# Kernel optimization log

Hardware: AMD Instinct MI355X
Metric: run time of the kernel (lower is better)

Reference implementation:

```python
import jax, jax.numpy as jnp
import numpy as np

C = 36   # num_classes
H = 256  # hidden_dim


def setup_inputs() -> dict:
    key = jax.random.key(0)
    ks = jax.random.split(key, 12)
    B, L, Dl, Dg = 32, 196, 1024, 1024
    s = lambda d: 1.0 / np.sqrt(d)
    return {
        "local_features": jax.random.normal(ks[0], (B, L, Dl), jnp.float32),
        "global_average_pool": jax.random.normal(ks[1], (B, Dg), jnp.float32),
        "Wl": jax.random.normal(ks[2], (Dl, C * H), jnp.float32) * s(Dl),
        "bl": jax.random.normal(ks[3], (C * H,), jnp.float32) * s(Dl),
        "Wg": jax.random.normal(ks[4], (Dg, C * H), jnp.float32) * s(Dg),
        "bg": jax.random.normal(ks[5], (C * H,), jnp.float32) * s(Dg),
        "Wh": jax.random.normal(ks[6], (H, H), jnp.float32) * s(H),
        "bh": jax.random.normal(ks[7], (H,), jnp.float32) * s(H),
        "Wr": jax.random.normal(ks[8], (H, 4), jnp.float32) * s(H),
        "br": jax.random.normal(ks[9], (4,), jnp.float32) * s(H),
        "Wc": jax.random.normal(ks[10], (H, 1), jnp.float32) * s(H),
        "bc": jax.random.normal(ks[11], (1,), jnp.float32) * s(H),
    }


def reference(local_features, global_average_pool, Wl, bl, Wg, bg, Wh, bh, Wr, br, Wc, bc):
    B, L, _ = local_features.shape
    # global projection -> [B, C, H]
    xg = (global_average_pool @ Wg + bg).reshape(B, C, H)
    # local projection -> [B, L, C, H] -> [B, C, L, H]
    xl = (local_features @ Wl + bl).reshape(B, L, C, H).transpose(0, 2, 1, 3)
    # per-class attention scores over locations: [B, C, L]
    dot = jnp.einsum('bch,bclh->bcl', xg, xl)
    attn = jax.nn.softmax(dot, axis=-1)
    # attention-weighted sum over locations: [B, C, H]
    ws = jnp.einsum('bcl,bclh->bch', attn, xl)
    hid = jax.nn.relu(ws @ Wh + bh)
    bbox_coords = (hid @ Wr + br).reshape(B, C * 4)   # [B, 4C]
    bbox_presence = (hid @ Wc + bc)[..., 0]           # [B, C]
    return bbox_coords, bbox_presence
```

## Files before the change

kernel.cpp:

```cpp
#include <hip/hip_runtime.h>
#include <hip/hip_bf16.h>
#include <stdint.h>

#define NCLS 36
#define HDIM 256
#define BSZ  32
#define LLOC 196
#define DIN  1024
#define NCH  9216

#define XG_N 294912
#define SC_N 225792
#define V_N  1179648

__global__ __launch_bounds__(256) void kB_xg_part(
    const float* __restrict__ Wg, const float* __restrict__ gap,
    float* __restrict__ xg_part) {
  __shared__ float4 gs[16][32];
  const int tid = threadIdx.x;
  const int n   = blockIdx.x * 256 + tid;
  const int kc  = blockIdx.y * 128;
  const int b0  = blockIdx.z * 16;

  for (int i = tid; i < 512; i += 256) {
    int bi = i >> 5, pos = i & 31;
    gs[bi][pos] = *(const float4*)&gap[(size_t)(b0 + bi) * DIN + kc + pos * 4];
  }
  __syncthreads();

  float acc[16] = {0,0,0,0,0,0,0,0,0,0,0,0,0,0,0,0};
  const float* wp = Wg + (size_t)kc * NCH + n;
  #pragma unroll 2
  for (int k4 = 0; k4 < 32; ++k4) {
    float w0 = wp[(size_t)(k4 * 4 + 0) * NCH];
    float w1 = wp[(size_t)(k4 * 4 + 1) * NCH];
    float w2 = wp[(size_t)(k4 * 4 + 2) * NCH];
    float w3 = wp[(size_t)(k4 * 4 + 3) * NCH];
    #pragma unroll
    for (int bi = 0; bi < 16; ++bi) {
      float4 g = gs[bi][k4];
      acc[bi] += g.x * w0 + g.y * w1 + g.z * w2 + g.w * w3;
    }
  }
  #pragma unroll
  for (int bi = 0; bi < 16; ++bi)
    xg_part[(size_t)blockIdx.y * XG_N + (size_t)(b0 + bi) * NCH + n] = acc[bi];
}

__global__ void kBr_xg(const float* __restrict__ xg_part,
                       const float* __restrict__ bg, float* __restrict__ xg) {
  int i = blockIdx.x * 256 + threadIdx.x;
  float s = bg[i % NCH];
  #pragma unroll
  for (int p = 0; p < 8; ++p) s += xg_part[(size_t)p * XG_N + i];
  xg[i] = s;
}

__global__ __launch_bounds__(256) void kC_V(
    const float* __restrict__ Wl, const float* __restrict__ xg,
    float* __restrict__ V) {
  __shared__ float4 xs[8][64];
  const int tid = threadIdx.x;
  const int c   = blockIdx.x;
  const int k   = blockIdx.y * 256 + tid;
  const int b0  = blockIdx.z * 8;

  for (int i = tid; i < 512; i += 256) {
    int bi = i >> 6, j = i & 63;
    xs[bi][j] = *(const float4*)&xg[(size_t)(b0 + bi) * NCH + c * HDIM + j * 4];
  }
  __syncthreads();

  float acc[8] = {0,0,0,0,0,0,0,0};
  const float* wl = Wl + (size_t)k * NCH + c * HDIM;
  #pragma unroll 2
  for (int j = 0; j < 64; ++j) {
    float4 w = *(const float4*)&wl[j * 4];
    #pragma unroll
    for (int bi = 0; bi < 8; ++bi) {
      float4 x = xs[bi][j];
      acc[bi] += w.x * x.x + w.y * x.y + w.z * x.z + w.w * x.w;
    }
  }
  #pragma unroll
  for (int bi = 0; bi < 8; ++bi)
    V[(size_t)((b0 + bi) * NCLS + c) * DIN + k] = acc[bi];
}

__global__ __launch_bounds__(256) void kD_scores(
    const float* __restrict__ local, const float* __restrict__ V,
    float* __restrict__ sc_part) {
  __shared__ float4 vs[12][32];
  const int tid = threadIdx.x;
  const int b   = blockIdx.x;
  const int cg  = blockIdx.y;
  const int ks  = blockIdx.z;

  for (int i = tid; i < 384; i += 256) {
    int ci = i >> 5, pos = i & 31;
    vs[ci][pos] = *(const float4*)&V[(size_t)(b * NCLS + cg * 12 + ci) * DIN
                                     + ks * 128 + pos * 4];
  }
  __syncthreads();

  const int l = tid;
  if (l >= LLOC) return;
  const float* lp = local + (size_t)(b * LLOC + l) * DIN + ks * 128;
  float acc[12] = {0,0,0,0,0,0,0,0,0,0,0,0};
  #pragma unroll 2
  for (int j = 0; j < 32; ++j) {
    float4 a = *(const float4*)&lp[j * 4];
    #pragma unroll
    for (int ci = 0; ci < 12; ++ci) {
      float4 v = vs[ci][j];
      acc[ci] += a.x * v.x + a.y * v.y + a.z * v.z + a.w * v.w;
    }
  }
  #pragma unroll
  for (int ci = 0; ci < 12; ++ci)
    sc_part[(size_t)ks * SC_N + (size_t)(b * NCLS + cg * 12 + ci) * LLOC + l] = acc[ci];
}

__global__ __launch_bounds__(64) void kE_softmax(
    const float* __restrict__ sc_part, float* __restrict__ attn2) {
  const int b = blockIdx.x, c = blockIdx.y, t = threadIdx.x;
  const size_t base = (size_t)(b * NCLS + c) * LLOC;
  float sc[4];
  int nl = 0;
  float m = -1e30f;
  for (int l = t; l < LLOC; l += 64) {
    float s = 0.f;
    #pragma unroll
    for (int p = 0; p < 8; ++p) s += sc_part[(size_t)p * SC_N + base + l];
    sc[nl++] = s; m = fmaxf(m, s);
  }
  #pragma unroll
  for (int off = 32; off >= 1; off >>= 1) m = fmaxf(m, __shfl_xor(m, off));
  float sum = 0.f;
  for (int i = 0; i < nl; ++i) { sc[i] = __expf(sc[i] - m); sum += sc[i]; }
  #pragma unroll
  for (int off = 32; off >= 1; off >>= 1) sum += __shfl_xor(sum, off);
  float inv = 1.0f / sum;
  nl = 0;
  for (int l = t; l < LLOC; l += 64) attn2[base + l] = sc[nl++] * inv;
}

__global__ __launch_bounds__(256) void kF_U(
    const float* __restrict__ local, const float* __restrict__ attn2,
    float* __restrict__ U) {
  __shared__ float4 as4[12][49];
  const int tid  = threadIdx.x;
  const int b    = blockIdx.x;
  const int k    = blockIdx.y * 128 + (tid & 127);
  const int half = __builtin_amdgcn_readfirstlane(tid >> 7);
  const int cb   = blockIdx.z * 12;

  for (int i = tid; i < 588; i += 256) {
    int ci = i / 49, pos = i - ci * 49;
    as4[ci][pos] = *(const float4*)&attn2[(size_t)(b * NCLS + cb + ci) * LLOC + pos * 4];
  }
  __syncthreads();

  float acc[6] = {0,0,0,0,0,0};
  const float* lp = local + (size_t)b * LLOC * DIN + k;
  #pragma unroll 2
  for (int l4 = 0; l4 < 49; ++l4) {
    float a0 = lp[(size_t)(l4 * 4 + 0) * DIN];
    float a1 = lp[(size_t)(l4 * 4 + 1) * DIN];
    float a2 = lp[(size_t)(l4 * 4 + 2) * DIN];
    float a3 = lp[(size_t)(l4 * 4 + 3) * DIN];
    #pragma unroll
    for (int ci = 0; ci < 6; ++ci) {
      float4 w = as4[half * 6 + ci][l4];
      acc[ci] += a0 * w.x + a1 * w.y + a2 * w.z + a3 * w.w;
    }
  }
  #pragma unroll
  for (int ci = 0; ci < 6; ++ci)
    U[(size_t)(b * NCLS + cb + half * 6 + ci) * DIN + k] = acc[ci];
}

__global__ __launch_bounds__(256) void kG_ws(
    const float* __restrict__ Wl, const float* __restrict__ U,
    float* __restrict__ wsh_part) {
  __shared__ float4 us[16][32];
  const int tid = threadIdx.x;
  const int c   = blockIdx.x;
  const int kc  = blockIdx.y * 128;
  const int b0  = blockIdx.z * 16;
  const int h   = tid;

  for (int i = tid; i < 512; i += 256) {
    int bi = i >> 5, pos = i & 31;
    us[bi][pos] = *(const float4*)&U[(size_t)((b0 + bi) * NCLS + c) * DIN + kc + pos * 4];
  }
  __syncthreads();

  float acc[16] = {0,0,0,0,0,0,0,0,0,0,0,0,0,0,0,0};
  const float* wp = Wl + (size_t)kc * NCH + c * HDIM + h;
  #pragma unroll 2
  for (int k4 = 0; k4 < 32; ++k4) {
    float w0 = wp[(size_t)(k4 * 4 + 0) * NCH];
    float w1 = wp[(size_t)(k4 * 4 + 1) * NCH];
    float w2 = wp[(size_t)(k4 * 4 + 2) * NCH];
    float w3 = wp[(size_t)(k4 * 4 + 3) * NCH];
    #pragma unroll
    for (int bi = 0; bi < 16; ++bi) {
      float4 u = us[bi][k4];
      acc[bi] += u.x * w0 + u.y * w1 + u.z * w2 + u.w * w3;
    }
  }
  const size_t base = (size_t)blockIdx.y * XG_N + c * HDIM + h;
  #pragma unroll
  for (int bi = 0; bi < 16; ++bi)
    wsh_part[base + (size_t)(b0 + bi) * NCH] = acc[bi];
}

__global__ __launch_bounds__(256) void kH_heads(
    const float* __restrict__ Wh, const float* __restrict__ bh,
    const float* __restrict__ Wr, const float* __restrict__ br,
    const float* __restrict__ Wc, const float* __restrict__ bc,
    const float* __restrict__ bl,
    const float* __restrict__ wsh_part, float* __restrict__ out) {
  __shared__ float ws_s[3][HDIM];
  __shared__ float hid_s[3][HDIM];
  const int b = blockIdx.x, c0 = blockIdx.y * 3;
  const int j = threadIdx.x;

  #pragma unroll
  for (int ci = 0; ci < 3; ++ci) {
    size_t base = (size_t)b * NCH + (c0 + ci) * HDIM + j;
    float s = bl[(c0 + ci) * HDIM + j];
    #pragma unroll
    for (int p = 0; p < 8; ++p) s += wsh_part[(size_t)p * XG_N + base];
    ws_s[ci][j] = s;
  }
  __syncthreads();

  float acc[3] = {0,0,0};
  for (int h = 0; h < HDIM; ++h) {
    float whj = Wh[(size_t)h * HDIM + j];
    acc[0] += ws_s[0][h] * whj;
    acc[1] += ws_s[1][h] * whj;
    acc[2] += ws_s[2][h] * whj;
  }
  float bj = bh[j];
  #pragma unroll
  for (int ci = 0; ci < 3; ++ci) hid_s[ci][j] = fmaxf(acc[ci] + bj, 0.0f);
  __syncthreads();

  const int r = j >> 6, j0 = j & 63;
  for (int ci = 0; ci < 3; ++ci) {
    const int c = c0 + ci;
    float s = 0.f;
    #pragma unroll
    for (int m = 0; m < 4; ++m)
      s += hid_s[ci][j0 + 64 * m] * Wr[(j0 + 64 * m) * 4 + r];
    #pragma unroll
    for (int off = 32; off >= 1; off >>= 1) s += __shfl_xor(s, off);
    if (j0 == 0) out[(size_t)b * (NCLS * 4) + c * 4 + r] = s + br[r];
    if (r == 0) {
      float p = 0.f;
      #pragma unroll
      for (int m = 0; m < 4; ++m)
        p += hid_s[ci][j0 + 64 * m] * Wc[j0 + 64 * m];
      #pragma unroll
      for (int off = 32; off >= 1; off >>= 1) p += __shfl_xor(p, off);
      if (j0 == 0) out[BSZ * NCLS * 4 + b * NCLS + c] = p + bc[0];
    }
  }
}

extern "C" void kernel_launch(void* const* d_in, const int* in_sizes, int n_in,
                              void* d_out, int out_size, void* d_ws, size_t ws_size,
                              hipStream_t stream) {
  const float* local = (const float*)d_in[0];
  const float* gap   = (const float*)d_in[1];
  const float* Wl    = (const float*)d_in[2];
  const float* bl    = (const float*)d_in[3];
  const float* Wg    = (const float*)d_in[4];
  const float* bg    = (const float*)d_in[5];
  const float* Wh    = (const float*)d_in[6];
  const float* bh    = (const float*)d_in[7];
  const float* Wr    = (const float*)d_in[8];
  const float* br    = (const float*)d_in[9];
  const float* Wc    = (const float*)d_in[10];
  const float* bc    = (const float*)d_in[11];
  float* out         = (float*)d_out;

  float* A  = (float*)d_ws;
  float* B  = A + (size_t)8 * XG_N;
  float* C  = B + XG_N;
  float* D  = C + V_N;
  float* E  = D + SC_N;

  kB_xg_part<<<dim3(36, 8, 2), dim3(256), 0, stream>>>(Wg, gap, A);
  kBr_xg   <<<dim3(XG_N / 256), dim3(256), 0, stream>>>(A, bg, B);
  kC_V     <<<dim3(36, 4, 4), dim3(256), 0, stream>>>(Wl, B, C);
  kD_scores<<<dim3(32, 3, 8), dim3(256), 0, stream>>>(local, C, A);
  kE_softmax<<<dim3(32, 36), dim3(64), 0, stream>>>(A, D);
  kF_U     <<<dim3(32, 8, 3), dim3(256), 0, stream>>>(local, D, E);
  kG_ws    <<<dim3(36, 8, 2), dim3(256), 0, stream>>>(Wl, E, A);
  kH_heads <<<dim3(32, 12), dim3(256), 0, stream>>>(Wh, bh, Wr, br, Wc, bc, bl, A, out);
}
```

Baseline: 268.7 us.

## Fold xg split-K reduction into kC_V and remap thread tiles to two outputs

Removes the separate kBr_xg reduction kernel by summing the eight split-K partials plus bias while kC_V loads its shared tile. Every GEMM-like kernel (xg, V, scores, U, ws) is re-tiled so each thread computes two output columns or rows over half as many batch or class entries. The aim is more independent global loads in flight per thread with the same accumulator count, and one fewer launch. kC_V now reads the partials redundantly across its blocks, and the extra loads raise register pressure.

```diff
diff --git a/kernel.cpp b/kernel.cpp
--- a/kernel.cpp
+++ b/kernel.cpp
@@ -8,121 +8,132 @@
 #define LLOC 196
 #define DIN  1024
 #define NCH  9216
-
 #define XG_N 294912
 #define SC_N 225792
 #define V_N  1179648
 
-__global__ __launch_bounds__(256) void kB_xg_part(
+__global__ __launch_bounds__(256) void kA_xg_part(
     const float* __restrict__ Wg, const float* __restrict__ gap,
-    float* __restrict__ xg_part) {
-  __shared__ float4 gs[16][32];
-  const int tid = threadIdx.x;
-  const int n   = blockIdx.x * 256 + tid;
-  const int kc  = blockIdx.y * 128;
-  const int b0  = blockIdx.z * 16;
-
+    float* __restrict__ A) {
+  __shared__ __align__(16) float4 gs[512];
+  const int tid = threadIdx.x;
+  const int nt = blockIdx.x, ks = blockIdx.y, bh = blockIdx.z;
+  const int kc = ks * 128, b0 = bh * 16;
   for (int i = tid; i < 512; i += 256) {
     int bi = i >> 5, pos = i & 31;
-    gs[bi][pos] = *(const float4*)&gap[(size_t)(b0 + bi) * DIN + kc + pos * 4];
-  }
-  __syncthreads();
-
-  float acc[16] = {0,0,0,0,0,0,0,0,0,0,0,0,0,0,0,0};
+    gs[bi * 32 + pos] = *(const float4*)&gap[(size_t)(b0 + bi) * DIN + kc + pos * 4];
+  }
+  __syncthreads();
+  const int g = tid >> 7, lane = tid & 127;
+  const int n = nt * 256 + lane;
+  float acc0[8] = {0,0,0,0,0,0,0,0};
+  float acc1[8] = {0,0,0,0,0,0,0,0};
   const float* wp = Wg + (size_t)kc * NCH + n;
-  #pragma unroll 2
   for (int k4 = 0; k4 < 32; ++k4) {
-    float w0 = wp[(size_t)(k4 * 4 + 0) * NCH];
-    float w1 = wp[(size_t)(k4 * 4 + 1) * NCH];
-    float w2 = wp[(size_t)(k4 * 4 + 2) * NCH];
-    float w3 = wp[(size_t)(k4 * 4 + 3) * NCH];
-    #pragma unroll
-    for (int bi = 0; bi < 16; ++bi) {
-      float4 g = gs[bi][k4];
-      acc[bi] += g.x * w0 + g.y * w1 + g.z * w2 + g.w * w3;
-    }
-  }
-  #pragma unroll
-  for (int bi = 0; bi < 16; ++bi)
-    xg_part[(size_t)blockIdx.y * XG_N + (size_t)(b0 + bi) * NCH + n] = acc[bi];
-}
-
-__global__ void kBr_xg(const float* __restrict__ xg_part,
-                       const float* __restrict__ bg, float* __restrict__ xg) {
-  int i = blockIdx.x * 256 + threadIdx.x;
-  float s = bg[i % NCH];
-  #pragma unroll
-  for (int p = 0; p < 8; ++p) s += xg_part[(size_t)p * XG_N + i];
-  xg[i] = s;
+    float w10 = wp[(size_t)(k4 * 4 + 0) * NCH];
+    float w11 = wp[(size_t)(k4 * 4 + 1) * NCH];
+    float w12 = wp[(size_t)(k4 * 4 + 2) * NCH];
+    float w13 = wp[(size_t)(k4 * 4 + 3) * NCH];
+    float w20 = wp[(size_t)(k4 * 4 + 0) * NCH + 128];
+    float w21 = wp[(size_t)(k4 * 4 + 1) * NCH + 128];
+    float w22 = wp[(size_t)(k4 * 4 + 2) * NCH + 128];
+    float w23 = wp[(size_t)(k4 * 4 + 3) * NCH + 128];
+    #pragma unroll
+    for (int bi = 0; bi < 8; ++bi) {
+      float4 gv = gs[(g * 8 + bi) * 32 + k4];
+      acc0[bi] += gv.x * w10 + gv.y * w11 + gv.z * w12 + gv.w * w13;
+      acc1[bi] += gv.x * w20 + gv.y * w21 + gv.z * w22 + gv.w * w23;
+    }
+  }
+  #pragma unroll
+  for (int bi = 0; bi < 8; ++bi) {
+    size_t o = (size_t)ks * XG_N + (size_t)(b0 + g * 8 + bi) * NCH + n;
+    A[o]       = acc0[bi];
+    A[o + 128] = acc1[bi];
+  }
 }
 
 __global__ __launch_bounds__(256) void kC_V(
-    const float* __restrict__ Wl, const float* __restrict__ xg,
-    float* __restrict__ V) {
-  __shared__ float4 xs[8][64];
-  const int tid = threadIdx.x;
-  const int c   = blockIdx.x;
-  const int k   = blockIdx.y * 256 + tid;
-  const int b0  = blockIdx.z * 8;
-
+    const float* __restrict__ Wl, const float* __restrict__ A,
+    const float* __restrict__ bg, float* __restrict__ V) {
+  __shared__ __align__(16) float4 xs[512];
+  const int tid = threadIdx.x;
+  const int c = blockIdx.x, kq = blockIdx.y, b0 = blockIdx.z * 8;
   for (int i = tid; i < 512; i += 256) {
     int bi = i >> 6, j = i & 63;
-    xs[bi][j] = *(const float4*)&xg[(size_t)(b0 + bi) * NCH + c * HDIM + j * 4];
-  }
-  __syncthreads();
-
-  float acc[8] = {0,0,0,0,0,0,0,0};
-  const float* wl = Wl + (size_t)k * NCH + c * HDIM;
-  #pragma unroll 2
+    size_t off = (size_t)(b0 + bi) * NCH + c * HDIM + j * 4;
+    float4 s = *(const float4*)&bg[c * HDIM + j * 4];
+    #pragma unroll
+    for (int p = 0; p < 8; ++p) {
+      float4 t = *(const float4*)&A[(size_t)p * XG_N + off];
+      s.x += t.x; s.y += t.y; s.z += t.z; s.w += t.w;
+    }
+    xs[bi * 64 + j] = s;
+  }
+  __syncthreads();
+  const int g = tid >> 7, lane = tid & 127;
+  const int k1 = kq * 256 + lane, k2 = k1 + 128;
+  float acc0[4] = {0,0,0,0};
+  float acc1[4] = {0,0,0,0};
+  const float* wl1 = Wl + (size_t)k1 * NCH + c * HDIM;
+  const float* wl2 = Wl + (size_t)k2 * NCH + c * HDIM;
   for (int j = 0; j < 64; ++j) {
-    float4 w = *(const float4*)&wl[j * 4];
-    #pragma unroll
-    for (int bi = 0; bi < 8; ++bi) {
-      float4 x = xs[bi][j];
-      acc[bi] += w.x * x.x + w.y * x.y + w.z * x.z + w.w * x.w;
-    }
-  }
-  #pragma unroll
-  for (int bi = 0; bi < 8; ++bi)
-    V[(size_t)((b0 + bi) * NCLS + c) * DIN + k] = acc[bi];
+    float4 w1 = *(const float4*)&wl1[j * 4];
+    float4 w2 = *(const float4*)&wl2[j * 4];
+    #pragma unroll
+    for (int bi = 0; bi < 4; ++bi) {
+      float4 x = xs[(g * 4 + bi) * 64 + j];
+      acc0[bi] += w1.x * x.x + w1.y * x.y + w1.z * x.z + w1.w * x.w;
+      acc1[bi] += w2.x * x.x + w2.y * x.y + w2.z * x.z + w2.w * x.w;
+    }
+  }
+  #pragma unroll
+  for (int bi = 0; bi < 4; ++bi) {
+    size_t o = (size_t)((b0 + g * 4 + bi) * NCLS + c) * DIN;
+    V[o + k1] = acc0[bi];
+    V[o + k2] = acc1[bi];
+  }
 }
 
 __global__ __launch_bounds__(256) void kD_scores(
-    const float* __restrict__ local, const float* __restrict__ V,
-    float* __restrict__ sc_part) {
-  __shared__ float4 vs[12][32];
-  const int tid = threadIdx.x;
-  const int b   = blockIdx.x;
-  const int cg  = blockIdx.y;
-  const int ks  = blockIdx.z;
-
+    const float* __restrict__ local_f, const float* __restrict__ V,
+    float* __restrict__ A) {
+  __shared__ __align__(16) float4 vs[384];
+  const int tid = threadIdx.x;
+  const int b = blockIdx.x, cg = blockIdx.y, ks = blockIdx.z;
   for (int i = tid; i < 384; i += 256) {
     int ci = i >> 5, pos = i & 31;
-    vs[ci][pos] = *(const float4*)&V[(size_t)(b * NCLS + cg * 12 + ci) * DIN
-                                     + ks * 128 + pos * 4];
-  }
-  __syncthreads();
-
-  const int l = tid;
-  if (l >= LLOC) return;
-  const float* lp = local + (size_t)(b * LLOC + l) * DIN + ks * 128;
-  float acc[12] = {0,0,0,0,0,0,0,0,0,0,0,0};
-  #pragma unroll 2
+    vs[ci * 32 + pos] = *(const float4*)&V[(size_t)(b * NCLS + cg * 12 + ci) * DIN
+                                           + ks * 128 + pos * 4];
+  }
+  __syncthreads();
+  const int g = tid >> 7, p = tid & 127;
+  if (p >= 98) return;
+  const int l1 = p, l2 = p + 98;
+  const float* lp1 = local_f + (size_t)(b * LLOC + l1) * DIN + ks * 128;
+  const float* lp2 = local_f + (size_t)(b * LLOC + l2) * DIN + ks * 128;
+  float acc0[6] = {0,0,0,0,0,0};
+  float acc1[6] = {0,0,0,0,0,0};
   for (int j = 0; j < 32; ++j) {
-    float4 a = *(const float4*)&lp[j * 4];
-    #pragma unroll
-    for (int ci = 0; ci < 12; ++ci) {
-      float4 v = vs[ci][j];
-      acc[ci] += a.x * v.x + a.y * v.y + a.z * v.z + a.w * v.w;
-    }
-  }
-  #pragma unroll
-  for (int ci = 0; ci < 12; ++ci)
-    sc_part[(size_t)ks * SC_N + (size_t)(b * NCLS + cg * 12 + ci) * LLOC + l] = acc[ci];
+    float4 a1 = *(const float4*)&lp1[j * 4];
+    float4 a2 = *(const float4*)&lp2[j * 4];
+    #pragma unroll
+    for (int ci = 0; ci < 6; ++ci) {
+      float4 v = vs[(g * 6 + ci) * 32 + j];
+      acc0[ci] += a1.x * v.x + a1.y * v.y + a1.z * v.z + a1.w * v.w;
+      acc1[ci] += a2.x * v.x + a2.y * v.y + a2.z * v.z + a2.w * v.w;
+    }
+  }
+  #pragma unroll
+  for (int ci = 0; ci < 6; ++ci) {
+    size_t o = (size_t)ks * SC_N + (size_t)(b * NCLS + cg * 12 + g * 6 + ci) * LLOC;
+    A[o + l1] = acc0[ci];
+    A[o + l2] = acc1[ci];
+  }
 }
 
 __global__ __launch_bounds__(64) void kE_softmax(
-    const float* __restrict__ sc_part, float* __restrict__ attn2) {
+    const float* __restrict__ A, float* __restrict__ attn2) {
   const int b = blockIdx.x, c = blockIdx.y, t = threadIdx.x;
   const size_t base = (size_t)(b * NCLS + c) * LLOC;
   float sc[4];
@@ -131,7 +142,7 @@
   for (int l = t; l < LLOC; l += 64) {
     float s = 0.f;
     #pragma unroll
-    for (int p = 0; p < 8; ++p) s += sc_part[(size_t)p * SC_N + base + l];
+    for (int p = 0; p < 8; ++p) s += A[(size_t)p * SC_N + base + l];
     sc[nl++] = s; m = fmaxf(m, s);
   }
   #pragma unroll
@@ -146,74 +157,87 @@
 }
 
 __global__ __launch_bounds__(256) void kF_U(
-    const float* __restrict__ local, const float* __restrict__ attn2,
+    const float* __restrict__ local_f, const float* __restrict__ attn2,
     float* __restrict__ U) {
-  __shared__ float4 as4[12][49];
-  const int tid  = threadIdx.x;
-  const int b    = blockIdx.x;
-  const int k    = blockIdx.y * 128 + (tid & 127);
-  const int half = __builtin_amdgcn_readfirstlane(tid >> 7);
-  const int cb   = blockIdx.z * 12;
-
+  __shared__ __align__(16) float4 as4[588];
+  const int tid = threadIdx.x;
+  const int b = blockIdx.x, ksf = blockIdx.y, cgf = blockIdx.z;
   for (int i = tid; i < 588; i += 256) {
     int ci = i / 49, pos = i - ci * 49;
-    as4[ci][pos] = *(const float4*)&attn2[(size_t)(b * NCLS + cb + ci) * LLOC + pos * 4];
-  }
-  __syncthreads();
-
-  float acc[6] = {0,0,0,0,0,0};
-  const float* lp = local + (size_t)b * LLOC * DIN + k;
-  #pragma unroll 2
+    as4[ci * 49 + pos] = *(const float4*)&attn2[(size_t)(b * NCLS + cgf * 12 + ci) * LLOC
+                                                + pos * 4];
+  }
+  __syncthreads();
+  const int q = tid >> 6, lane = tid & 63;
+  const int k1 = ksf * 128 + lane, k2 = k1 + 64;
+  const int cb = q * 3;
+  float acc0[3] = {0,0,0};
+  float acc1[3] = {0,0,0};
+  const float* lp1 = local_f + (size_t)b * LLOC * DIN + k1;
+  const float* lp2 = lp1 + 64;
   for (int l4 = 0; l4 < 49; ++l4) {
-    float a0 = lp[(size_t)(l4 * 4 + 0) * DIN];
-    float a1 = lp[(size_t)(l4 * 4 + 1) * DIN];
-    float a2 = lp[(size_t)(l4 * 4 + 2) * DIN];
-    float a3 = lp[(size_t)(l4 * 4 + 3) * DIN];
-    #pragma unroll
-    for (int ci = 0; ci < 6; ++ci) {
-      float4 w = as4[half * 6 + ci][l4];
-      acc[ci] += a0 * w.x + a1 * w.y + a2 * w.z + a3 * w.w;
-    }
-  }
-  #pragma unroll
-  for (int ci = 0; ci < 6; ++ci)
-    U[(size_t)(b * NCLS + cb + half * 6 + ci) * DIN + k] = acc[ci];
+    float a10 = lp1[(size_t)(l4 * 4 + 0) * DIN];
+    float a11 = lp1[(size_t)(l4 * 4 + 1) * DIN];
+    float a12 = lp1[(size_t)(l4 * 4 + 2) * DIN];
+    float a13 = lp1[(size_t)(l4 * 4 + 3) * DIN];
+    float a20 = lp2[(size_t)(l4 * 4 + 0) * DIN];
+    float a21 = lp2[(size_t)(l4 * 4 + 1) * DIN];
+    float a22 = lp2[(size_t)(l4 * 4 + 2) * DIN];
+    float a23 = lp2[(size_t)(l4 * 4 + 3) * DIN];
+    #pragma unroll
+    for (int ci = 0; ci < 3; ++ci) {
+      float4 w = as4[(cb + ci) * 49 + l4];
+      acc0[ci] += a10 * w.x + a11 * w.y + a12 * w.z + a13 * w.w;
+      acc1[ci] += a20 * w.x + a21 * w.y + a22 * w.z + a23 * w.w;
+    }
+  }
+  #pragma unroll
+  for (int ci = 0; ci < 3; ++ci) {
+    size_t o = (size_t)(b * NCLS + cgf * 12 + cb + ci) * DIN;
+    U[o + k1] = acc0[ci];
+    U[o + k2] = acc1[ci];
+  }
 }
 
 __global__ __launch_bounds__(256) void kG_ws(
     const float* __restrict__ Wl, const float* __restrict__ U,
-    float* __restrict__ wsh_part) {
-  __shared__ float4 us[16][32];
-  const int tid = threadIdx.x;
-  const int c   = blockIdx.x;
-  const int kc  = blockIdx.y * 128;
-  const int b0  = blockIdx.z * 16;
-  const int h   = tid;
-
+    float* __restrict__ A) {
+  __shared__ __align__(16) float4 us[512];
+  const int tid = threadIdx.x;
+  const int c = blockIdx.x, ksg = blockIdx.y, b0 = blockIdx.z * 16;
+  const int kc = ksg * 128;
   for (int i = tid; i < 512; i += 256) {
     int bi = i >> 5, pos = i & 31;
-    us[bi][pos] = *(const float4*)&U[(size_t)((b0 + bi) * NCLS + c) * DIN + kc + pos * 4];
-  }
-  __syncthreads();
-
-  float acc[16] = {0,0,0,0,0,0,0,0,0,0,0,0,0,0,0,0};
-  const float* wp = Wl + (size_t)kc * NCH + c * HDIM + h;
-  #pragma unroll 2
+    us[bi * 32 + pos] = *(const float4*)&U[(size_t)((b0 + bi) * NCLS + c) * DIN
+                                           + kc + pos * 4];
+  }
+  __syncthreads();
+  const int g = tid >> 7, lane = tid & 127;
+  float acc0[8] = {0,0,0,0,0,0,0,0};
+  float acc1[8] = {0,0,0,0,0,0,0,0};
+  const float* wp = Wl + (size_t)kc * NCH + c * HDIM + lane;
   for (int k4 = 0; k4 < 32; ++k4) {
-    float w0 = wp[(size_t)(k4 * 4 + 0) * NCH];
-    float w1 = wp[(size_t)(k4 * 4 + 1) * NCH];
-    float w2 = wp[(size_t)(k4 * 4 + 2) * NCH];
-    float w3 = wp[(size_t)(k4 * 4 + 3) * NCH];
-    #pragma unroll
-    for (int bi = 0; bi < 16; ++bi) {
-      float4 u = us[bi][k4];
-      acc[bi] += u.x * w0 + u.y * w1 + u.z * w2 + u.w * w3;
-    }
-  }
-  const size_t base = (size_t)blockIdx.y * XG_N + c * HDIM + h;
-  #pragma unroll
-  for (int bi = 0; bi < 16; ++bi)
-    wsh_part[base + (size_t)(b0 + bi) * NCH] = acc[bi];
+    float w10 = wp[(size_t)(k4 * 4 + 0) * NCH];
+    float w11 = wp[(size_t)(k4 * 4 + 1) * NCH];
+    float w12 = wp[(size_t)(k4 * 4 + 2) * NCH];
+    float w13 = wp[(size_t)(k4 * 4 + 3) * NCH];
+    float w20 = wp[(size_t)(k4 * 4 + 0) * NCH + 128];
+    float w21 = wp[(size_t)(k4 * 4 + 1) * NCH + 128];
+    float w22 = wp[(size_t)(k4 * 4 + 2) * NCH + 128];
+    float w23 = wp[(size_t)(k4 * 4 + 3) * NCH + 128];
+    #pragma unroll
+    for (int bi = 0; bi < 8; ++bi) {
+      float4 u = us[(g * 8 + bi) * 32 + k4];
+      acc0[bi] += u.x * w10 + u.y * w11 + u.z * w12 + u.w * w13;
+      acc1[bi] += u.x * w20 + u.y * w21 + u.z * w22 + u.w * w23;
+    }
+  }
+  #pragma unroll
+  for (int bi = 0; bi < 8; ++bi) {
+    size_t o = (size_t)ksg * XG_N + (size_t)(b0 + g * 8 + bi) * NCH + c * HDIM + lane;
+    A[o]       = acc0[bi];
+    A[o + 128] = acc1[bi];
+  }
 }
 
 __global__ __launch_bounds__(256) void kH_heads(
@@ -221,22 +245,20 @@
     const float* __restrict__ Wr, const float* __restrict__ br,
     const float* __restrict__ Wc, const float* __restrict__ bc,
     const float* __restrict__ bl,
-    const float* __restrict__ wsh_part, float* __restrict__ out) {
+    const float* __restrict__ A, float* __restrict__ out) {
   __shared__ float ws_s[3][HDIM];
   __shared__ float hid_s[3][HDIM];
   const int b = blockIdx.x, c0 = blockIdx.y * 3;
   const int j = threadIdx.x;
-
   #pragma unroll
   for (int ci = 0; ci < 3; ++ci) {
     size_t base = (size_t)b * NCH + (c0 + ci) * HDIM + j;
     float s = bl[(c0 + ci) * HDIM + j];
     #pragma unroll
-    for (int p = 0; p < 8; ++p) s += wsh_part[(size_t)p * XG_N + base];
+    for (int p = 0; p < 8; ++p) s += A[(size_t)p * XG_N + base];
     ws_s[ci][j] = s;
   }
   __syncthreads();
-
   float acc[3] = {0,0,0};
   for (int h = 0; h < HDIM; ++h) {
     float whj = Wh[(size_t)h * HDIM + j];
@@ -248,7 +270,6 @@
   #pragma unroll
   for (int ci = 0; ci < 3; ++ci) hid_s[ci][j] = fmaxf(acc[ci] + bj, 0.0f);
   __syncthreads();
-
   const int r = j >> 6, j0 = j & 63;
   for (int ci = 0; ci < 3; ++ci) {
     const int c = c0 + ci;
@@ -288,18 +309,16 @@
   const float* bc    = (const float*)d_in[11];
   float* out         = (float*)d_out;
 
-  float* A  = (float*)d_ws;
-  float* B  = A + (size_t)8 * XG_N;
-  float* C  = B + XG_N;
-  float* D  = C + V_N;
-  float* E  = D + SC_N;
-
-  kB_xg_part<<<dim3(36, 8, 2), dim3(256), 0, stream>>>(Wg, gap, A);
-  kBr_xg   <<<dim3(XG_N / 256), dim3(256), 0, stream>>>(A, bg, B);
-  kC_V     <<<dim3(36, 4, 4), dim3(256), 0, stream>>>(Wl, B, C);
-  kD_scores<<<dim3(32, 3, 8), dim3(256), 0, stream>>>(local, C, A);
-  kE_softmax<<<dim3(32, 36), dim3(64), 0, stream>>>(A, D);
-  kF_U     <<<dim3(32, 8, 3), dim3(256), 0, stream>>>(local, D, E);
-  kG_ws    <<<dim3(36, 8, 2), dim3(256), 0, stream>>>(Wl, E, A);
-  kH_heads <<<dim3(32, 12), dim3(256), 0, stream>>>(Wh, bh, Wr, br, Wc, bc, bl, A, out);
-}
+  float* A     = (float*)d_ws;
+  float* V     = A + (size_t)8 * XG_N;
+  float* attn2 = V + V_N;
+  float* U     = attn2 + SC_N;
+
+  kA_xg_part<<<dim3(36, 8, 2), dim3(256), 0, stream>>>(Wg, gap, A);
+  kC_V      <<<dim3(36, 4, 4), dim3(256), 0, stream>>>(Wl, A, bg, V);
+  kD_scores <<<dim3(32, 3, 8), dim3(256), 0, stream>>>(local, V, A);
+  kE_softmax<<<dim3(32, 36),   dim3(64),  0, stream>>>(A, attn2);
+  kF_U      <<<dim3(32, 8, 3), dim3(256), 0, stream>>>(local, attn2, U);
+  kG_ws     <<<dim3(36, 8, 2), dim3(256), 0, stream>>>(Wl, U, A);
+  kH_heads  <<<dim3(32, 12),   dim3(256), 0, stream>>>(Wh, bh, Wr, br, Wc, bc, bl, A, out);
+}
```

New measurement: 296.3 us. 1.1x slower.
